# Optimization experiments

Measured on AMD Instinct MI355X. Metric: run time of the kernel, lower is better.

## Reference

```python
import jax, jax.numpy as jnp
import numpy as np
from jax import lax

B, C, H, W = 16, 64, 64, 64
K = 3                  # kernel_size
D_IN = C * K           # moe input dim = 192
D_OUT = 128            # out_channels
N_EXP = 8
TOP_K = 2
N_SHARED = 1


def setup_inputs() -> dict:
    key = jax.random.key(0)
    ks = jax.random.split(key, 7)
    x = jax.random.normal(ks[0], (B, C, H, W), dtype=jnp.float32)
    # depthwise conv: groups=C, each input channel -> K output channels
    conv_w = jax.random.normal(ks[1], (D_IN, 1, K, K), dtype=jnp.float32) * 0.1
    router_w = jax.random.normal(ks[2], (D_IN, N_EXP), dtype=jnp.float32) * 0.05
    w_experts = jax.random.normal(ks[3], (N_EXP, D_IN, D_OUT), dtype=jnp.float32) * 0.05
    b_experts = jnp.zeros((N_EXP, D_OUT), dtype=jnp.float32)
    w_shared = jax.random.normal(ks[4], (N_SHARED, D_IN, D_OUT), dtype=jnp.float32) * 0.05
    b_shared = jnp.zeros((N_SHARED, D_OUT), dtype=jnp.float32)
    return {"x": x, "conv_w": conv_w, "router_w": router_w,
            "w_experts": w_experts, "b_experts": b_experts,
            "w_shared": w_shared, "b_shared": b_shared}


def _moe_conv2d(x, conv_w, router_w, w_experts, b_experts, w_shared, b_shared):
    pad = K // 2
    # depthwise conv (B,C,H,W) -> (B, C*K, H, W)
    x_conv = lax.conv_general_dilated(
        x, conv_w, window_strides=(1, 1), padding=[(pad, pad), (pad, pad)],
        feature_group_count=C, dimension_numbers=("NCHW", "OIHW", "NCHW"))
    # flatten to token stream (B*H*W, D_IN)
    tokens = x_conv.transpose(0, 2, 3, 1).reshape(-1, D_IN)
    # router: softmax probs, top-k gating renormalized over selected experts
    logits = tokens @ router_w                       # (T, E)
    probs = jax.nn.softmax(logits, axis=-1)
    top_v, top_i = lax.top_k(probs, TOP_K)           # (T, k)
    gates = top_v / jnp.sum(top_v, axis=-1, keepdims=True)
    # all-expert outputs then gather the selected k per token
    expert_out = jnp.einsum("ti,eio->teo", tokens, w_experts) + b_experts  # (T, E, O)
    sel = jnp.take_along_axis(expert_out, top_i[:, :, None], axis=1)       # (T, k, O)
    y_flat = jnp.einsum("tk,tko->to", gates, sel)
    # shared experts applied to every token
    shared = jnp.einsum("ti,sio->tso", tokens, w_shared) + b_shared        # (T, S, O)
    y_flat = y_flat + jnp.sum(shared, axis=1)
    # back to feature map (B, O, H, W)
    return y_flat.reshape(B, H, W, D_OUT).transpose(0, 3, 1, 2)


def reference(x, conv_w, router_w, w_experts, b_experts, w_shared, b_shared):
    return _moe_conv2d(x, conv_w, router_w, w_experts, b_experts, w_shared, b_shared)
```

## Files before the change

### kernel.cpp

```cpp
#include <hip/hip_runtime.h>
#include <math.h>

#define BB   16
#define CC   64
#define DIN  192
#define DOUT 128
#define NEXP 8
#define NMAT 9
#define NTOK 65536
#define CAP  65568
#define SLABROWS 65552

#define TOKSTRIDE 200
#define LOGSTRIDE 9
#define CSTRIDE 136

typedef short bf16x8 __attribute__((ext_vector_type(8)));
typedef float f32x4  __attribute__((ext_vector_type(4)));

#define WS_TOK   0u
#define WS_WT    25165824u
#define WS_CNT   25608192u
#define WS_RT    25608256u
#define WS_RG    27706432u
#define WS_SLAB  29804608u
#define WS_TOTAL  63367232u
#define WS_TOTAL3 80148544u

__device__ __forceinline__ unsigned short f2bf(float f) {
    union { float f; unsigned u; } v; v.f = f;
    unsigned u = v.u;
    u += 0x7fffu + ((u >> 16) & 1u);
    return (unsigned short)(u >> 16);
}
__device__ __forceinline__ float bf2f(unsigned short s) {
    union { unsigned u; float f; } v; v.u = ((unsigned)s) << 16;
    return v.f;
}

__global__ __launch_bounds__(256)
void k1a_conv(const float* __restrict__ x,
              const float* __restrict__ conv_w,
              const float* __restrict__ router_w,
              const float* __restrict__ w_experts,
              const float* __restrict__ w_shared,
              unsigned short* __restrict__ tokbuf,
              unsigned short* __restrict__ wt,
              int* __restrict__ cnt,
              int* __restrict__ rowtok, float* __restrict__ rowgate)
{
    __shared__ __attribute__((aligned(16))) unsigned short tokbf[64 * TOKSTRIDE];
    __shared__ float logits[64 * LOGSTRIDE];
    __shared__ int lcnt[8];
    __shared__ int lbase[8];

    const int tid = threadIdx.x;
    const int bh  = blockIdx.x;
    const int b   = bh >> 6;
    const int h   = bh & 63;

    for (int idx = tid; idx < 64 * LOGSTRIDE; idx += 256) logits[idx] = 0.f;
    if (tid < 8) lcnt[tid] = 0;
    __syncthreads();

    {
        int idx = bh * 192 + tid;
        if (tid < 192) {
            int e = idx / 24576, rem = idx - e * 24576;
            int n = rem / DIN,  k  = rem - n * DIN;
            wt[idx] = f2bf(w_experts[(size_t)e * 24576 + k * DOUT + n]
                           + w_shared[k * DOUT + n]);
        }
    }

    const int   h0  = (h > 0)  ? (h - 1) : 0;
    const int   h2  = (h < 63) ? (h + 1) : 63;
    const float mh0 = (h > 0)  ? 1.f : 0.f;
    const float mh2 = (h < 63) ? 1.f : 0.f;

    const int w = tid & 63;
    const int q = __builtin_amdgcn_readfirstlane(tid >> 6);

    const int   wm  = (w == 0)  ? 0  : (w - 1);
    const int   wp  = (w == 63) ? 63 : (w + 1);
    const float mwm = (w == 0)  ? 0.f : 1.f;
    const float mwp = (w == 63) ? 0.f : 1.f;

    float lacc[8];
    #pragma unroll
    for (int e = 0; e < 8; ++e) lacc[e] = 0.f;

    const float* xb = x + (size_t)b * CC * 4096;

    #pragma unroll 2
    for (int i = 0; i < 16; ++i) {
        const int c = q * 16 + i;
        const float* xc = xb + (size_t)c * 4096;
        const float* r0 = xc + h0 * 64;
        const float* r1 = xc + h  * 64;
        const float* r2 = xc + h2 * 64;
        float x00 = r0[wm], x01 = r0[w], x02 = r0[wp];
        float x10 = r1[wm], x11 = r1[w], x12 = r1[wp];
        float x20 = r2[wm], x21 = r2[w], x22 = r2[wp];
        x00 *= mh0 * mwm; x01 *= mh0; x02 *= mh0 * mwp;
        x10 *= mwm;                    x12 *= mwp;
        x20 *= mh2 * mwm; x21 *= mh2; x22 *= mh2 * mwp;

        #pragma unroll
        for (int j = 0; j < 3; ++j) {
            const int f = 3 * c + j;
            const float* w9  = conv_w + f * 9;
            const float* rwf = router_w + f * 8;
            float acc = x00 * w9[0] + x01 * w9[1] + x02 * w9[2]
                      + x10 * w9[3] + x11 * w9[4] + x12 * w9[5]
                      + x20 * w9[6] + x21 * w9[7] + x22 * w9[8];
            tokbf[w * TOKSTRIDE + f] = f2bf(acc);
            #pragma unroll
            for (int e = 0; e < 8; ++e) lacc[e] += acc * rwf[e];
        }
    }

    #pragma unroll
    for (int e = 0; e < 8; ++e)
        atomicAdd(&logits[w * LOGSTRIDE + e], lacc[e]);
    __syncthreads();

    int e0 = 0, e1 = -1, r0k = 0, r1k = 0;
    float g0 = 0.f, g1 = 0.f;
    if (tid < 64) {
        float l[8];
        #pragma unroll
        for (int e = 0; e < 8; ++e) l[e] = logits[tid * LOGSTRIDE + e];
        float l0 = l[0];
        #pragma unroll
        for (int e = 1; e < 8; ++e) if (l[e] > l0) { l0 = l[e]; e0 = e; }
        float l1 = -INFINITY;
        #pragma unroll
        for (int e = 0; e < 8; ++e) {
            if (e == e0) continue;
            if (l[e] > l1) { l1 = l[e]; e1 = e; }
        }
        g0 = 1.f / (1.f + expf(l1 - l0));
        g1 = 1.f - g0;
        r0k = atomicAdd(&lcnt[e0], 1);
        r1k = atomicAdd(&lcnt[e1], 1);
    }
    __syncthreads();
    if (tid < 8) lbase[tid] = atomicAdd(&cnt[tid], lcnt[tid]);
    __syncthreads();
    if (tid < 64) {
        int t   = bh * 64 + tid;
        int p0i = e0 * CAP + lbase[e0] + r0k;
        int p1i = e1 * CAP + lbase[e1] + r1k;
        rowtok[p0i]  = t;
        rowgate[p0i] = g0;
        rowtok[p1i]  = t | (1 << 20);
        rowgate[p1i] = g1;
    }

    for (int idx = tid; idx < 1536; idx += 256) {
        int row = idx / 24, seg = idx - row * 24;
        *(bf16x8*)(tokbuf + (size_t)(bh * 64 + row) * 192 + seg * 8) =
            *(const bf16x8*)(tokbf + row * TOKSTRIDE + seg * 8);
    }
}

__global__ __launch_bounds__(256)
void k4_all(const unsigned short* __restrict__ tokbuf,
            const unsigned short* __restrict__ wt,
            const float* __restrict__ b_experts,
            const float* __restrict__ b_shared,
            const int* __restrict__ cnt,
            const int* __restrict__ rowtok, const float* __restrict__ rowgate,
            unsigned short* __restrict__ slab)
{
    __shared__ __attribute__((aligned(16))) unsigned short atile[2][16 * TOKSTRIDE];
    __shared__ __attribute__((aligned(16))) unsigned short ctile[2][16 * CSTRIDE];
    __shared__ int   stok[2][16];
    __shared__ float sgate[2][16];

    const int tid  = threadIdx.x;
    const int e    = blockIdx.x >> 8;
    const int jb   = blockIdx.x & 255;
    const int jstep = 256;

    const int wave = tid >> 6;
    const int lane = tid & 63;
    const int m16  = lane & 15, quad = lane >> 4;
    const int o0   = (wave * 2 + 0) * 16 + m16;
    const int o1   = (wave * 2 + 1) * 16 + m16;

    const unsigned short* wb = wt + (size_t)e * DOUT * DIN;
    bf16x8 bfr0[6], bfr1[6];
    #pragma unroll
    for (int ks = 0; ks < 6; ++ks) {
        bfr0[ks] = *(const bf16x8*)(wb + (size_t)o0 * DIN + ks * 32 + quad * 8);
        bfr1[ks] = *(const bf16x8*)(wb + (size_t)o1 * DIN + ks * 32 + quad * 8);
    }
    const float be0 = b_experts[e * DOUT + o0] + b_shared[o0];
    const float be1 = b_experts[e * DOUT + o1] + b_shared[o1];

    const int cnt_e  = cnt[e];
    const int ntiles = (cnt_e + 15) >> 4;
    const int*   rt = rowtok  + e * CAP;
    const float* rg = rowgate + e * CAP;

    const int r0i = tid / 24,         s0i = tid - r0i * 24;
    const int r1i = (tid + 256) / 24, s1i = (tid + 256) - r1i * 24;
    const bool has1 = (tid + 256) < 384;

    #define FETCH_RAW(r) (((r) < cnt_e) ? rt[r] : NTOK)
    #define FETCH_G(r)   (((r) < cnt_e) ? rg[r] : 0.f)

    if (jb < ntiles) {
        int base = jb * 16;
        if (tid < 16) {
            stok[0][tid]  = FETCH_RAW(base + tid);
            sgate[0][tid] = FETCH_G(base + tid);
        }
        {
            int rawa = FETCH_RAW(base + r0i);
            *(bf16x8*)&atile[0][r0i * TOKSTRIDE + s0i * 8] =
                *(const bf16x8*)(tokbuf + (size_t)(rawa & 0x1FFFF) * 192 + s0i * 8);
            if (has1) {
                int rawb = FETCH_RAW(base + r1i);
                *(bf16x8*)&atile[0][r1i * TOKSTRIDE + s1i * 8] =
                    *(const bf16x8*)(tokbuf + (size_t)(rawb & 0x1FFFF) * 192 + s1i * 8);
            }
        }
    }
    __syncthreads();

    int buf = 0;
    for (int j = jb; j < ntiles; j += jstep, buf ^= 1) {
        const int jn = j + jstep;
        const bool more = (jn < ntiles);

        bf16x8 nx0 = {0,0,0,0,0,0,0,0}, nx1 = {0,0,0,0,0,0,0,0};
        int nmt = NTOK; float nmg = 0.f;
        if (more) {
            int base = jn * 16;
            if (tid < 16) { nmt = FETCH_RAW(base + tid); nmg = FETCH_G(base + tid); }
            int rawa = FETCH_RAW(base + r0i);
            nx0 = *(const bf16x8*)(tokbuf + (size_t)(rawa & 0x1FFFF) * 192 + s0i * 8);
            if (has1) {
                int rawb = FETCH_RAW(base + r1i);
                nx1 = *(const bf16x8*)(tokbuf + (size_t)(rawb & 0x1FFFF) * 192 + s1i * 8);
            }
        }

        bf16x8 a[6];
        #pragma unroll
        for (int ks = 0; ks < 6; ++ks)
            a[ks] = *(const bf16x8*)&atile[buf][m16 * TOKSTRIDE + ks * 32 + quad * 8];

        f32x4 acc0 = {0.f, 0.f, 0.f, 0.f};
        f32x4 acc1 = {0.f, 0.f, 0.f, 0.f};
        #pragma unroll
        for (int ks = 0; ks < 6; ++ks) {
            acc0 = __builtin_amdgcn_mfma_f32_16x16x32_bf16(a[ks], bfr0[ks], acc0, 0, 0, 0);
            acc1 = __builtin_amdgcn_mfma_f32_16x16x32_bf16(a[ks], bfr1[ks], acc1, 0, 0, 0);
        }

        #pragma unroll
        for (int i = 0; i < 4; ++i) {
            int   row = quad * 4 + i;
            float g   = sgate[buf][row];
            ctile[buf][row * CSTRIDE + o0] = f2bf(g * (acc0[i] + be0));
            ctile[buf][row * CSTRIDE + o1] = f2bf(g * (acc1[i] + be1));
        }

        if (more) {
            if (tid < 16) { stok[buf ^ 1][tid] = nmt; sgate[buf ^ 1][tid] = nmg; }
            *(bf16x8*)&atile[buf ^ 1][r0i * TOKSTRIDE + s0i * 8] = nx0;
            if (has1) *(bf16x8*)&atile[buf ^ 1][r1i * TOKSTRIDE + s1i * 8] = nx1;
        }
        __syncthreads();

        {
            int row = tid >> 4, chk = tid & 15;
            int raw = stok[buf][row];
            int t    = raw & 0x1FFFF;
            int slot = raw >> 20;
            *(bf16x8*)(slab + (size_t)slot * SLABROWS * DOUT
                            + (size_t)t * DOUT + chk * 8) =
                *(const bf16x8*)&ctile[buf][row * CSTRIDE + chk * 8];
        }
    }
    #undef FETCH_RAW
    #undef FETCH_G
}

__global__ __launch_bounds__(256)
void k3_combine(const unsigned short* __restrict__ slab,
                float* __restrict__ out)
{
    __shared__ float out_lds[32 * 129];

    const int tid = threadIdx.x;
    const int bid = blockIdx.x;
    const int bh  = bid >> 1;
    const int wh  = bid & 1;
    const int b   = bh >> 6;
    const int h   = bh & 63;
    const int t0  = bh * 64 + wh * 32;

    const unsigned short* s0 = slab;
    const unsigned short* s1 = slab + (size_t)SLABROWS * DOUT;

    #pragma unroll
    for (int it = 0; it < 2; ++it) {
        int idx = it * 256 + tid;
        int tl = idx >> 4, chk = idx & 15;
        size_t gt = (size_t)t0 + tl;
        bf16x8 v0 = *(const bf16x8*)(s0 + gt * DOUT + chk * 8);
        bf16x8 v1 = *(const bf16x8*)(s1 + gt * DOUT + chk * 8);
        float* dst = &out_lds[tl * 129 + chk * 8];
        #pragma unroll
        for (int q = 0; q < 8; ++q)
            dst[q] = bf2f((unsigned short)v0[q]) + bf2f((unsigned short)v1[q]);
    }
    __syncthreads();

    float* outp = out + ((size_t)b * DOUT) * 4096 + h * 64 + wh * 32;
    for (int idx = tid; idx < 32 * DOUT; idx += 256) {
        int wloc = idx & 31, o = idx >> 5;
        outp[(size_t)o * 4096 + wloc] = out_lds[wloc * 129 + o];
    }
}

#define OUTSTRIDE 129
#define MAXROWS 320
#define MAXTILES 20

__global__ __launch_bounds__(256)
void moe_conv2d_mfma(const float* __restrict__ x,
                     const float* __restrict__ conv_w,
                     const float* __restrict__ router_w,
                     const unsigned short* __restrict__ wt,
                     const float* __restrict__ b_experts,
                     const float* __restrict__ b_shared,
                     float* __restrict__ out)
{
    __shared__ __attribute__((aligned(16))) unsigned short tokbf[64 * TOKSTRIDE];
    __shared__ float out_lds[64 * OUTSTRIDE];
    __shared__ float rw[DIN * NEXP];
    __shared__ float logits[64 * LOGSTRIDE];
    __shared__ float sg0[64], sg1[64];
    __shared__ int   se0[64], se1[64];
    __shared__ int   rowtok[MAXROWS];
    __shared__ float rowgate[MAXROWS];
    __shared__ int   cbuf[NMAT];
    __shared__ int   tilexp[MAXTILES], tilebase[MAXTILES];
    __shared__ int   ntiles_s;

    const int tid = threadIdx.x;
    const int bh  = blockIdx.x;
    const int b   = bh >> 6;
    const int h   = bh & 63;

    for (int idx = tid; idx < DIN * NEXP; idx += 256) rw[idx] = router_w[idx];
    for (int idx = tid; idx < 64 * LOGSTRIDE; idx += 256) logits[idx] = 0.f;
    __syncthreads();
    {
        const int w  = tid & 63;
        const int fq = tid >> 6;
        float lacc[8];
        #pragma unroll
        for (int e = 0; e < 8; ++e) lacc[e] = 0.f;
        for (int i = 0; i < 48; ++i) {
            int f = i * 4 + fq;
            int c = f / 3;
            const float* wp    = conv_w + f * 9;
            const float* xbase = x + ((size_t)(b * 64 + c) * 64) * 64;
            float acc = 0.f;
            #pragma unroll
            for (int kh = 0; kh < 3; ++kh) {
                int hh = h + kh - 1;
                if (hh < 0 || hh > 63) continue;
                const float* xrow = xbase + hh * 64;
                #pragma unroll
                for (int kw = 0; kw < 3; ++kw) {
                    int ww = w + kw - 1;
                    if (ww < 0 || ww > 63) continue;
                    acc += xrow[ww] * wp[kh * 3 + kw];
                }
            }
            tokbf[w * TOKSTRIDE + f] = f2bf(acc);
            const float* rwf = rw + f * 8;
            #pragma unroll
            for (int e = 0; e < 8; ++e) lacc[e] += acc * rwf[e];
        }
        #pragma unroll
        for (int e = 0; e < 8; ++e)
            atomicAdd(&logits[w * LOGSTRIDE + e], lacc[e]);
    }
    __syncthreads();
    if (tid < 64) {
        int w = tid;
        float l[8];
        #pragma unroll
        for (int e = 0; e < 8; ++e) l[e] = logits[w * LOGSTRIDE + e];
        int e0 = 0; float l0 = l[0];
        #pragma unroll
        for (int e = 1; e < 8; ++e) if (l[e] > l0) { l0 = l[e]; e0 = e; }
        int e1 = -1; float l1 = -INFINITY;
        #pragma unroll
        for (int e = 0; e < 8; ++e) {
            if (e == e0) continue;
            if (l[e] > l1) { l1 = l[e]; e1 = e; }
        }
        float g0 = 1.f / (1.f + expf(l1 - l0));
        sg0[w] = g0; sg1[w] = 1.f - g0;
        se0[w] = e0; se1[w] = e1;
    }
    __syncthreads();
    for (int idx = tid; idx < 64 * DOUT; idx += 256) {
        int t = idx >> 7, o = idx & 127;
        out_lds[t * OUTSTRIDE + o] = b_shared[o]
            + sg0[t] * b_experts[se0[t] * DOUT + o]
            + sg1[t] * b_experts[se1[t] * DOUT + o];
    }
    if (tid < 8) {
        int c = 0;
        for (int t = 0; t < 64; ++t) c += (se0[t] == tid) + (se1[t] == tid);
        cbuf[tid] = c;
    } else if (tid == 8) cbuf[8] = 64;
    __syncthreads();
    if (tid < NMAT) {
        int e = tid;
        int start = 0, tb = 0;
        for (int e2 = 0; e2 < e; ++e2) {
            int ce = cbuf[e2];
            int tl = (ce + 15) >> 4;
            start += tl << 4; tb += tl;
        }
        int ce = cbuf[e];
        int tl = (ce + 15) >> 4;
        for (int j = 0; j < tl; ++j) { tilexp[tb + j] = e; tilebase[tb + j] = start + (j << 4); }
        if (e == 8) ntiles_s = tb + tl;
        int j = 0;
        if (e < 8) {
            for (int t = 0; t < 64; ++t) {
                if (se0[t] == e) { rowtok[start + j] = t; rowgate[start + j] = sg0[t]; ++j; }
                if (se1[t] == e) { rowtok[start + j] = t; rowgate[start + j] = sg1[t]; ++j; }
            }
        } else {
            for (int t = 0; t < 64; ++t) { rowtok[start + j] = t; rowgate[start + j] = 1.f; ++j; }
        }
        for (; j < (tl << 4); ++j) { rowtok[start + j] = 0; rowgate[start + j] = 0.f; }
    }
    __syncthreads();
    {
        const int wave = tid >> 6;
        const int lane = tid & 63;
        const int m16  = lane & 15;
        const int quad = lane >> 4;
        const int nt   = ntiles_s;
        for (int ti = wave; ti < nt; ti += 4) {
            int e    = tilexp[ti];
            int base = tilebase[ti];
            int tA = rowtok[base + m16];
            bf16x8 a[6];
            #pragma unroll
            for (int ks = 0; ks < 6; ++ks)
                a[ks] = *(const bf16x8*)(tokbf + tA * TOKSTRIDE + ks * 32 + quad * 8);
            int st[4]; float sgt[4];
            #pragma unroll
            for (int i2 = 0; i2 < 4; ++i2) {
                int r = base + quad * 4 + i2;
                st[i2] = rowtok[r]; sgt[i2] = rowgate[r];
            }
            const unsigned short* we = wt + (size_t)e * DOUT * DIN;
            for (int n = 0; n < 8; ++n) {
                const unsigned short* wp = we + (size_t)(n * 16 + m16) * DIN + quad * 8;
                f32x4 acc = {0.f, 0.f, 0.f, 0.f};
                #pragma unroll
                for (int ks = 0; ks < 6; ++ks) {
                    bf16x8 bfr2 = *(const bf16x8*)(wp + ks * 32);
                    acc = __builtin_amdgcn_mfma_f32_16x16x32_bf16(a[ks], bfr2, acc, 0, 0, 0);
                }
                int ncol = n * 16 + m16;
                #pragma unroll
                for (int i2 = 0; i2 < 4; ++i2)
                    atomicAdd(&out_lds[st[i2] * OUTSTRIDE + ncol], sgt[i2] * acc[i2]);
            }
        }
    }
    __syncthreads();
    {
        float* outp = out + (((size_t)b * DOUT) * 64 + h) * 64;
        for (int idx = tid; idx < 64 * DOUT; idx += 256) {
            int w = idx & 63, o = idx >> 6;
            outp[(size_t)o * 4096 + w] = out_lds[w * OUTSTRIDE + o];
        }
    }
}

__global__ __launch_bounds__(256)
void prep_weights_only(const float* __restrict__ w_experts,
                       const float* __restrict__ w_shared,
                       unsigned short* __restrict__ wt)
{
    int e = blockIdx.x;
    const float* src = (e < 8) ? (w_experts + (size_t)e * DIN * DOUT) : w_shared;
    unsigned short* dst = wt + (size_t)e * DOUT * DIN;
    for (int idx = threadIdx.x; idx < DOUT * DIN; idx += 256) {
        int n = idx / DIN, k = idx - n * DIN;
        dst[idx] = f2bf(src[k * DOUT + n]);
    }
}

extern "C" void kernel_launch(void* const* d_in, const int* in_sizes, int n_in,
                              void* d_out, int out_size, void* d_ws, size_t ws_size,
                              hipStream_t stream)
{
    const float* x         = (const float*)d_in[0];
    const float* conv_w    = (const float*)d_in[1];
    const float* router_w  = (const float*)d_in[2];
    const float* w_experts = (const float*)d_in[3];
    const float* b_experts = (const float*)d_in[4];
    const float* w_shared  = (const float*)d_in[5];
    const float* b_shared  = (const float*)d_in[6];
    float* out = (float*)d_out;
    char* ws = (char*)d_ws;

    if (ws_size >= WS_TOTAL) {
        unsigned short* tokbuf  = (unsigned short*)(ws + WS_TOK);
        unsigned short* wt      = (unsigned short*)(ws + WS_WT);
        int*            cnt     = (int*)(ws + WS_CNT);
        int*            rowtok  = (int*)(ws + WS_RT);
        float*          rowgate = (float*)(ws + WS_RG);
        unsigned short* slab    = (unsigned short*)(ws + WS_SLAB);

        hipMemsetAsync(cnt, 0, 16 * sizeof(int), stream);
        k1a_conv<<<dim3(1024), dim3(256), 0, stream>>>(
            x, conv_w, router_w, w_experts, w_shared,
            tokbuf, wt, cnt, rowtok, rowgate);
        k4_all<<<dim3(2048), dim3(256), 0, stream>>>(
            tokbuf, wt, b_experts, b_shared, cnt, rowtok, rowgate, slab);
        k3_combine<<<dim3(2048), dim3(256), 0, stream>>>(slab, out);
    } else {
        unsigned short* wt = (unsigned short*)ws;
        prep_weights_only<<<dim3(NMAT), dim3(256), 0, stream>>>(w_experts, w_shared, wt);
        moe_conv2d_mfma<<<dim3(1024), dim3(256), 0, stream>>>(
            x, conv_w, router_w, wt, b_experts, b_shared, out);
    }
}
```

Baseline: 149.0 us.

## Replace global expert dispatch and slab combine with per-row local MoE kernel

Drops the global per-expert token lists, memset, slab buffer and separate combine kernel. The conv kernel now writes only per-token gates and expert ids. A new kernel per image row loads its 64 tokens into LDS, buckets them by expert locally, runs MFMA tiles per expert, and accumulates gated results in LDS before writing the transposed output. This removes the slab round trip through global memory and one launch. In exchange, expert weights are reloaded from global/L2 per tile instead of held in registers, and the local grouping leaves partially filled tiles.

```diff
diff --git a/kernel.cpp b/kernel.cpp
--- a/kernel.cpp
+++ b/kernel.cpp
@@ -8,24 +8,17 @@
 #define NEXP 8
 #define NMAT 9
 #define NTOK 65536
-#define CAP  65568
-#define SLABROWS 65552
 
 #define TOKSTRIDE 200
 #define LOGSTRIDE 9
-#define CSTRIDE 136
 
 typedef short bf16x8 __attribute__((ext_vector_type(8)));
 typedef float f32x4  __attribute__((ext_vector_type(4)));
 
 #define WS_TOK   0u
 #define WS_WT    25165824u
-#define WS_CNT   25608192u
-#define WS_RT    25608256u
-#define WS_RG    27706432u
-#define WS_SLAB  29804608u
-#define WS_TOTAL  63367232u
-#define WS_TOTAL3 80148544u
+#define WS_TI    25608192u
+#define WS_TOTAL 26656768u
 
 __device__ __forceinline__ unsigned short f2bf(float f) {
     union { float f; unsigned u; } v; v.f = f;
@@ -46,13 +39,10 @@
               const float* __restrict__ w_shared,
               unsigned short* __restrict__ tokbuf,
               unsigned short* __restrict__ wt,
-              int* __restrict__ cnt,
-              int* __restrict__ rowtok, float* __restrict__ rowgate)
+              float* __restrict__ tokinfo)
 {
     __shared__ __attribute__((aligned(16))) unsigned short tokbf[64 * TOKSTRIDE];
     __shared__ float logits[64 * LOGSTRIDE];
-    __shared__ int lcnt[8];
-    __shared__ int lbase[8];
 
     const int tid = threadIdx.x;
     const int bh  = blockIdx.x;
@@ -60,7 +50,6 @@
     const int h   = bh & 63;
 
     for (int idx = tid; idx < 64 * LOGSTRIDE; idx += 256) logits[idx] = 0.f;
-    if (tid < 8) lcnt[tid] = 0;
     __syncthreads();
 
     {
@@ -125,37 +114,24 @@
         atomicAdd(&logits[w * LOGSTRIDE + e], lacc[e]);
     __syncthreads();
 
-    int e0 = 0, e1 = -1, r0k = 0, r1k = 0;
-    float g0 = 0.f, g1 = 0.f;
     if (tid < 64) {
         float l[8];
         #pragma unroll
         for (int e = 0; e < 8; ++e) l[e] = logits[tid * LOGSTRIDE + e];
-        float l0 = l[0];
+        int e0 = 0; float l0 = l[0];
         #pragma unroll
         for (int e = 1; e < 8; ++e) if (l[e] > l0) { l0 = l[e]; e0 = e; }
-        float l1 = -INFINITY;
+        int e1 = -1; float l1 = -INFINITY;
         #pragma unroll
         for (int e = 0; e < 8; ++e) {
             if (e == e0) continue;
             if (l[e] > l1) { l1 = l[e]; e1 = e; }
         }
-        g0 = 1.f / (1.f + expf(l1 - l0));
-        g1 = 1.f - g0;
-        r0k = atomicAdd(&lcnt[e0], 1);
-        r1k = atomicAdd(&lcnt[e1], 1);
-    }
-    __syncthreads();
-    if (tid < 8) lbase[tid] = atomicAdd(&cnt[tid], lcnt[tid]);
-    __syncthreads();
-    if (tid < 64) {
-        int t   = bh * 64 + tid;
-        int p0i = e0 * CAP + lbase[e0] + r0k;
-        int p1i = e1 * CAP + lbase[e1] + r1k;
-        rowtok[p0i]  = t;
-        rowgate[p0i] = g0;
-        rowtok[p1i]  = t | (1 << 20);
-        rowgate[p1i] = g1;
+        float g0 = 1.f / (1.f + expf(l1 - l0));
+        float4 v;
+        v.x = g0; v.y = 1.f - g0;
+        v.z = __int_as_float(e0); v.w = __int_as_float(e1);
+        *(float4*)(tokinfo + (size_t)(bh * 64 + tid) * 4) = v;
     }
 
     for (int idx = tid; idx < 1536; idx += 256) {
@@ -166,166 +142,115 @@
 }
 
 __global__ __launch_bounds__(256)
-void k4_all(const unsigned short* __restrict__ tokbuf,
+void k2_moe(const unsigned short* __restrict__ tokbuf,
             const unsigned short* __restrict__ wt,
             const float* __restrict__ b_experts,
             const float* __restrict__ b_shared,
-            const int* __restrict__ cnt,
-            const int* __restrict__ rowtok, const float* __restrict__ rowgate,
-            unsigned short* __restrict__ slab)
+            const float* __restrict__ tokinfo,
+            float* __restrict__ out)
 {
-    __shared__ __attribute__((aligned(16))) unsigned short atile[2][16 * TOKSTRIDE];
-    __shared__ __attribute__((aligned(16))) unsigned short ctile[2][16 * CSTRIDE];
-    __shared__ int   stok[2][16];
-    __shared__ float sgate[2][16];
-
-    const int tid  = threadIdx.x;
-    const int e    = blockIdx.x >> 8;
-    const int jb   = blockIdx.x & 255;
-    const int jstep = 256;
-
-    const int wave = tid >> 6;
-    const int lane = tid & 63;
-    const int m16  = lane & 15, quad = lane >> 4;
-    const int o0   = (wave * 2 + 0) * 16 + m16;
-    const int o1   = (wave * 2 + 1) * 16 + m16;
-
-    const unsigned short* wb = wt + (size_t)e * DOUT * DIN;
-    bf16x8 bfr0[6], bfr1[6];
-    #pragma unroll
-    for (int ks = 0; ks < 6; ++ks) {
-        bfr0[ks] = *(const bf16x8*)(wb + (size_t)o0 * DIN + ks * 32 + quad * 8);
-        bfr1[ks] = *(const bf16x8*)(wb + (size_t)o1 * DIN + ks * 32 + quad * 8);
-    }
-    const float be0 = b_experts[e * DOUT + o0] + b_shared[o0];
-    const float be1 = b_experts[e * DOUT + o1] + b_shared[o1];
-
-    const int cnt_e  = cnt[e];
-    const int ntiles = (cnt_e + 15) >> 4;
-    const int*   rt = rowtok  + e * CAP;
-    const float* rg = rowgate + e * CAP;
-
-    const int r0i = tid / 24,         s0i = tid - r0i * 24;
-    const int r1i = (tid + 256) / 24, s1i = (tid + 256) - r1i * 24;
-    const bool has1 = (tid + 256) < 384;
-
-    #define FETCH_RAW(r) (((r) < cnt_e) ? rt[r] : NTOK)
-    #define FETCH_G(r)   (((r) < cnt_e) ? rg[r] : 0.f)
-
-    if (jb < ntiles) {
-        int base = jb * 16;
-        if (tid < 16) {
-            stok[0][tid]  = FETCH_RAW(base + tid);
-            sgate[0][tid] = FETCH_G(base + tid);
-        }
-        {
-            int rawa = FETCH_RAW(base + r0i);
-            *(bf16x8*)&atile[0][r0i * TOKSTRIDE + s0i * 8] =
-                *(const bf16x8*)(tokbuf + (size_t)(rawa & 0x1FFFF) * 192 + s0i * 8);
-            if (has1) {
-                int rawb = FETCH_RAW(base + r1i);
-                *(bf16x8*)&atile[0][r1i * TOKSTRIDE + s1i * 8] =
-                    *(const bf16x8*)(tokbuf + (size_t)(rawb & 0x1FFFF) * 192 + s1i * 8);
-            }
-        }
-    }
-    __syncthreads();
-
-    int buf = 0;
-    for (int j = jb; j < ntiles; j += jstep, buf ^= 1) {
-        const int jn = j + jstep;
-        const bool more = (jn < ntiles);
-
-        bf16x8 nx0 = {0,0,0,0,0,0,0,0}, nx1 = {0,0,0,0,0,0,0,0};
-        int nmt = NTOK; float nmg = 0.f;
-        if (more) {
-            int base = jn * 16;
-            if (tid < 16) { nmt = FETCH_RAW(base + tid); nmg = FETCH_G(base + tid); }
-            int rawa = FETCH_RAW(base + r0i);
-            nx0 = *(const bf16x8*)(tokbuf + (size_t)(rawa & 0x1FFFF) * 192 + s0i * 8);
-            if (has1) {
-                int rawb = FETCH_RAW(base + r1i);
-                nx1 = *(const bf16x8*)(tokbuf + (size_t)(rawb & 0x1FFFF) * 192 + s1i * 8);
-            }
-        }
-
-        bf16x8 a[6];
-        #pragma unroll
-        for (int ks = 0; ks < 6; ++ks)
-            a[ks] = *(const bf16x8*)&atile[buf][m16 * TOKSTRIDE + ks * 32 + quad * 8];
-
-        f32x4 acc0 = {0.f, 0.f, 0.f, 0.f};
-        f32x4 acc1 = {0.f, 0.f, 0.f, 0.f};
-        #pragma unroll
-        for (int ks = 0; ks < 6; ++ks) {
-            acc0 = __builtin_amdgcn_mfma_f32_16x16x32_bf16(a[ks], bfr0[ks], acc0, 0, 0, 0);
-            acc1 = __builtin_amdgcn_mfma_f32_16x16x32_bf16(a[ks], bfr1[ks], acc1, 0, 0, 0);
-        }
-
-        #pragma unroll
-        for (int i = 0; i < 4; ++i) {
-            int   row = quad * 4 + i;
-            float g   = sgate[buf][row];
-            ctile[buf][row * CSTRIDE + o0] = f2bf(g * (acc0[i] + be0));
-            ctile[buf][row * CSTRIDE + o1] = f2bf(g * (acc1[i] + be1));
-        }
-
-        if (more) {
-            if (tid < 16) { stok[buf ^ 1][tid] = nmt; sgate[buf ^ 1][tid] = nmg; }
-            *(bf16x8*)&atile[buf ^ 1][r0i * TOKSTRIDE + s0i * 8] = nx0;
-            if (has1) *(bf16x8*)&atile[buf ^ 1][r1i * TOKSTRIDE + s1i * 8] = nx1;
-        }
-        __syncthreads();
-
-        {
-            int row = tid >> 4, chk = tid & 15;
-            int raw = stok[buf][row];
-            int t    = raw & 0x1FFFF;
-            int slot = raw >> 20;
-            *(bf16x8*)(slab + (size_t)slot * SLABROWS * DOUT
-                            + (size_t)t * DOUT + chk * 8) =
-                *(const bf16x8*)&ctile[buf][row * CSTRIDE + chk * 8];
-        }
-    }
-    #undef FETCH_RAW
-    #undef FETCH_G
-}
-
-__global__ __launch_bounds__(256)
-void k3_combine(const unsigned short* __restrict__ slab,
-                float* __restrict__ out)
-{
-    __shared__ float out_lds[32 * 129];
+    __shared__ __attribute__((aligned(16))) unsigned short tokbf[64 * TOKSTRIDE];
+    __shared__ float out_lds[64 * 129];
+    __shared__ float bsum[NEXP * DOUT];
+    __shared__ int   rowtok[256];
+    __shared__ float rowgate[256];
+    __shared__ int   lcnt[8], lstart[8];
+    __shared__ int   tilexp[16], tilebase[16];
+    __shared__ int   ntiles_s;
 
     const int tid = threadIdx.x;
-    const int bid = blockIdx.x;
-    const int bh  = bid >> 1;
-    const int wh  = bid & 1;
+    const int bh  = blockIdx.x;
     const int b   = bh >> 6;
     const int h   = bh & 63;
-    const int t0  = bh * 64 + wh * 32;
-
-    const unsigned short* s0 = slab;
-    const unsigned short* s1 = slab + (size_t)SLABROWS * DOUT;
-
-    #pragma unroll
-    for (int it = 0; it < 2; ++it) {
-        int idx = it * 256 + tid;
-        int tl = idx >> 4, chk = idx & 15;
-        size_t gt = (size_t)t0 + tl;
-        bf16x8 v0 = *(const bf16x8*)(s0 + gt * DOUT + chk * 8);
-        bf16x8 v1 = *(const bf16x8*)(s1 + gt * DOUT + chk * 8);
-        float* dst = &out_lds[tl * 129 + chk * 8];
-        #pragma unroll
-        for (int q = 0; q < 8; ++q)
-            dst[q] = bf2f((unsigned short)v0[q]) + bf2f((unsigned short)v1[q]);
-    }
-    __syncthreads();
-
-    float* outp = out + ((size_t)b * DOUT) * 4096 + h * 64 + wh * 32;
-    for (int idx = tid; idx < 32 * DOUT; idx += 256) {
-        int wloc = idx & 31, o = idx >> 5;
-        outp[(size_t)o * 4096 + wloc] = out_lds[wloc * 129 + o];
+    const size_t t0 = (size_t)bh * 64;
+
+    for (int idx = tid; idx < 1536; idx += 256) {
+        int row = idx / 24, seg = idx - row * 24;
+        *(bf16x8*)&tokbf[row * TOKSTRIDE + seg * 8] =
+            *(const bf16x8*)(tokbuf + (t0 + row) * 192 + seg * 8);
+    }
+    for (int idx = tid; idx < NEXP * DOUT; idx += 256)
+        bsum[idx] = b_experts[idx] + b_shared[idx & 127];
+    if (tid < 8) lcnt[tid] = 0;
+    for (int idx = tid; idx < 64 * 129; idx += 256) out_lds[idx] = 0.f;
+    __syncthreads();
+
+    int e0 = 0, e1 = 0, r0 = 0, r1 = 0;
+    float g0 = 0.f, g1 = 0.f;
+    if (tid < 64) {
+        float4 ti = *(const float4*)(tokinfo + (t0 + tid) * 4);
+        g0 = ti.x; g1 = ti.y;
+        e0 = __float_as_int(ti.z); e1 = __float_as_int(ti.w);
+        r0 = atomicAdd(&lcnt[e0], 1);
+        r1 = atomicAdd(&lcnt[e1], 1);
+    }
+    __syncthreads();
+    if (tid == 0) {
+        int start = 0, tb = 0;
+        for (int e = 0; e < 8; ++e) {
+            lstart[e] = start;
+            int tl = (lcnt[e] + 15) >> 4;
+            for (int j = 0; j < tl; ++j) {
+                tilexp[tb + j] = e; tilebase[tb + j] = start + (j << 4);
+            }
+            start += tl << 4; tb += tl;
+        }
+        ntiles_s = tb;
+    }
+    __syncthreads();
+    if (tid < 64) {
+        int p0 = lstart[e0] + r0, p1 = lstart[e1] + r1;
+        rowtok[p0] = tid; rowgate[p0] = g0;
+        rowtok[p1] = tid; rowgate[p1] = g1;
+    }
+    if (tid < 8) {
+        int e = tid, tl = (lcnt[e] + 15) >> 4;
+        for (int j = lcnt[e]; j < (tl << 4); ++j) {
+            rowtok[lstart[e] + j] = 0; rowgate[lstart[e] + j] = 0.f;
+        }
+    }
+    __syncthreads();
+
+    const int wave = tid >> 6, lane = tid & 63;
+    const int m16  = lane & 15, quad = lane >> 4;
+    const int nt   = ntiles_s;
+    for (int ti = 0; ti < nt; ++ti) {
+        int e = tilexp[ti], base = tilebase[ti];
+        int tA = rowtok[base + m16];
+        bf16x8 a[6];
+        #pragma unroll
+        for (int ks = 0; ks < 6; ++ks)
+            a[ks] = *(const bf16x8*)&tokbf[tA * TOKSTRIDE + ks * 32 + quad * 8];
+        int st[4]; float sg[4];
+        #pragma unroll
+        for (int i = 0; i < 4; ++i) {
+            int r = base + quad * 4 + i;
+            st[i] = rowtok[r]; sg[i] = rowgate[r];
+        }
+        const unsigned short* we = wt + (size_t)e * DOUT * DIN;
+        #pragma unroll
+        for (int nb2 = 0; nb2 < 2; ++nb2) {
+            int o = (wave * 2 + nb2) * 16 + m16;
+            const unsigned short* wp = we + (size_t)o * DIN + quad * 8;
+            f32x4 acc = {0.f, 0.f, 0.f, 0.f};
+            #pragma unroll
+            for (int ks = 0; ks < 6; ++ks) {
+                bf16x8 bfr = *(const bf16x8*)(wp + ks * 32);
+                acc = __builtin_amdgcn_mfma_f32_16x16x32_bf16(a[ks], bfr, acc, 0, 0, 0);
+            }
+            float be = bsum[e * DOUT + o];
+            #pragma unroll
+            for (int i = 0; i < 4; ++i)
+                if (sg[i] != 0.f)
+                    out_lds[st[i] * 129 + o] += sg[i] * (acc[i] + be);
+        }
+    }
+    __syncthreads();
+
+    float* outp = out + ((size_t)b * DOUT) * 4096 + h * 64;
+    for (int idx = tid; idx < 64 * DOUT; idx += 256) {
+        int w = idx & 63, o = idx >> 6;
+        outp[(size_t)o * 4096 + w] = out_lds[w * 129 + o];
     }
 }
 
@@ -528,18 +453,12 @@
     if (ws_size >= WS_TOTAL) {
         unsigned short* tokbuf  = (unsigned short*)(ws + WS_TOK);
         unsigned short* wt      = (unsigned short*)(ws + WS_WT);
-        int*            cnt     = (int*)(ws + WS_CNT);
-        int*            rowtok  = (int*)(ws + WS_RT);
-        float*          rowgate = (float*)(ws + WS_RG);
-        unsigned short* slab    = (unsigned short*)(ws + WS_SLAB);
-
-        hipMemsetAsync(cnt, 0, 16 * sizeof(int), stream);
+        float*          tokinfo = (float*)(ws + WS_TI);
+
         k1a_conv<<<dim3(1024), dim3(256), 0, stream>>>(
-            x, conv_w, router_w, w_experts, w_shared,
-            tokbuf, wt, cnt, rowtok, rowgate);
-        k4_all<<<dim3(2048), dim3(256), 0, stream>>>(
-            tokbuf, wt, b_experts, b_shared, cnt, rowtok, rowgate, slab);
-        k3_combine<<<dim3(2048), dim3(256), 0, stream>>>(slab, out);
+            x, conv_w, router_w, w_experts, w_shared, tokbuf, wt, tokinfo);
+        k2_moe<<<dim3(1024), dim3(256), 0, stream>>>(
+            tokbuf, wt, b_experts, b_shared, tokinfo, out);
     } else {
         unsigned short* wt = (unsigned short*)ws;
         prep_weights_only<<<dim3(NMAT), dim3(256), 0, stream>>>(w_experts, w_shared, wt);
```

After: 184.1 us. +23.6%, slower.
